# Kernel tuning notes

Measured on AMD Instinct MI355X. Metric: run time of the kernel, lower is better.

## Reference

```python
import jax, jax.numpy as jnp
import numpy as np

V, E = 1024, 2048
IN_DIM = OUT_DIM = 256
H = 4
D = OUT_DIM // H           # head_dim = 64
ENC = 8                    # causal_encoding_dim
HID = 32                   # causal_gate_hidden
LN_EPS = 1e-5


def setup_inputs() -> dict:
    key = jax.random.key(0)
    ks = jax.random.split(key, 12)
    s = 0.05
    return {
        "h": jax.random.normal(ks[0], (V, IN_DIM), jnp.float32),
        "causal_effects": jax.random.normal(ks[1], (V, V, 2), jnp.float32),
        "W": jax.random.normal(ks[2], (IN_DIM, OUT_DIM), jnp.float32) * s,
        "attn_w": jax.random.normal(ks[3], (2 * D + ENC,), jnp.float32) * s,
        "enc_w": jax.random.normal(ks[4], (2, ENC), jnp.float32) * s,
        "enc_b": jnp.zeros((ENC,), jnp.float32),
        "g1_w": jax.random.normal(ks[5], (2, HID), jnp.float32) * s,
        "g1_b": jnp.zeros((HID,), jnp.float32),
        "g2_w": jax.random.normal(ks[6], (HID, 1), jnp.float32) * s,
        "g2_b": jnp.zeros((1,), jnp.float32),
        "ln_g": jnp.ones((OUT_DIM,), jnp.float32),
        "ln_b": jnp.zeros((OUT_DIM,), jnp.float32),
        "incidence": jax.random.randint(ks[7], (V, E), 0, 2, dtype=jnp.int32),
    }


def _chan_forward(h, causal_effects, W, attn_w, enc_w, enc_b,
                  g1_w, g1_b, g2_w, g2_b, ln_g, ln_b, incidence):
    num_v, num_e = incidence.shape
    M = (incidence > 0).astype(h.dtype)                 # [V,E] binary membership
    mask = incidence > 0                                 # [V,E] bool

    Wh = h @ W                                           # [V,O]
    Whh = Wh.reshape(num_v, H, D)                        # [V,H,D]

    cnt_e = M.sum(axis=0)                                # [E] edge sizes
    deg_e = jnp.maximum(cnt_e, 1.0)
    h_bar = (M.T @ Wh) / deg_e[:, None]                  # [E,O] edge means
    hbh = h_bar.reshape(num_e, H, D)                     # [E,H,D]

    # number of "other" members for each (v,e): |e| - [v in e]
    n_ve = cnt_e[None, :] - M                            # [V,E]
    inv_n = jnp.where(n_ve > 0, 1.0 / jnp.maximum(n_ve, 1.0), 0.0)

    # per-(v,e) mean causal effect over other members of e
    diag_ce = jnp.diagonal(causal_effects, axis1=0, axis2=1).T   # [V,2]
    S = jnp.einsum('vuk,ue->vek', causal_effects, M)             # sum over members
    S = S - M[:, :, None] * diag_ce[:, None, :]                  # exclude u==v
    ce_mean = S * inv_n[:, :, None]                              # [V,E,2] (0 if no others)

    c = ce_mean @ enc_w + enc_b                                  # [V,E,ENC]

    a_v, a_e, a_c = attn_w[:D], attn_w[D:2 * D], attn_w[2 * D:]
    scores = (jnp.einsum('vhd,d->vh', Whh, a_v)[:, None, :]
              + jnp.einsum('ehd,d->eh', hbh, a_e)[None, :, :]
              + (c @ a_c)[:, :, None])                           # [V,E,H]
    scores = jax.nn.leaky_relu(scores, 0.2)
    neg = jnp.asarray(-1e9, scores.dtype)
    scores = jnp.where(mask[:, :, None], scores, neg)
    alpha = jax.nn.softmax(scores, axis=1) * mask[:, :, None].astype(scores.dtype)
    ap = alpha * inv_n[:, :, None]                               # alpha / n_others

    # causal gate psi(v,u) in [0,1], per vertex pair
    z = jax.nn.relu(causal_effects @ g1_w + g1_b)                # [V,V,HID]
    G = jax.nn.sigmoid((z @ g2_w)[..., 0] + g2_b[0])             # [V,V]

    # spread attention over edge members: A[v,u,h] = sum_e ap[v,e,h] * M[u,e]
    A = jnp.einsum('veh,ue->vuh', ap, M)                         # [V,V,H]
    out = jnp.einsum('vuh,vu,uhd->vhd', A, G, Whh)               # gated messages
    # remove self-contribution (u == v)
    s_v = ap.sum(axis=1)                                         # [V,H]
    Gvv = jnp.diagonal(G)                                        # [V]
    out = out - s_v[:, :, None] * Gvv[:, None, None] * Whh       # [V,H,D]

    out = out.reshape(num_v, -1) + Wh                            # residual (in==out dim)
    mu = out.mean(axis=-1, keepdims=True)
    var = out.var(axis=-1, keepdims=True)
    out = (out - mu) / jnp.sqrt(var + LN_EPS) * ln_g + ln_b
    return out                                                   # dropout = identity (eval)


def reference(h, causal_effects, W, attn_w, enc_w, enc_b,
              g1_w, g1_b, g2_w, g2_b, ln_g, ln_b, incidence):
    return _chan_forward(h, causal_effects, W, attn_w, enc_w, enc_b,
                         g1_w, g1_b, g2_w, g2_b, ln_g, ln_b, incidence)
```

## Files before the change

### kernel.cpp

```cpp
#include <hip/hip_runtime.h>
#include <hip/hip_bf16.h>

#define NV 1024
#define NE 2048

typedef unsigned short u16;
typedef unsigned char u8;
typedef unsigned long long u64;
typedef __attribute__((ext_vector_type(8))) short bf16x8;
typedef __attribute__((ext_vector_type(4))) float f32x4;
typedef __attribute__((ext_vector_type(16))) float f32x16;
typedef __attribute__((ext_vector_type(2))) long i64x2;

__device__ __forceinline__ float bf2f(u16 u) { return __uint_as_float(((unsigned)u) << 16); }
__device__ __forceinline__ u16 f2bf(float f) {
  unsigned x = __float_as_uint(f);
  return (u16)((x + 0x7fffu + ((x >> 16) & 1u)) >> 16);
}
__device__ __forceinline__ u8 f2fp8(float f) {
  unsigned x = __float_as_uint(f);
  unsigned sgn = (x >> 24) & 0x80;
  float af = __uint_as_float(x & 0x7fffffff);
  unsigned q;
  if (af >= 448.f) {
    q = 0x7e;
  } else if (af < 0.015625f) {
    q = (unsigned)rintf(af * 512.f);
  } else {
    unsigned xa = x & 0x7fffffff;
    xa += 0x7ffff + ((xa >> 20) & 1);
    q = (xa >> 20) - 960;
    if (q > 0x7e) q = 0x7e;
  }
  return (u8)(sgn | q);
}

#define GLL(src, dst)                                                        \
  __builtin_amdgcn_global_load_lds(                                          \
      (const __attribute__((address_space(1))) void*)(src),                  \
      (__attribute__((address_space(3))) void*)(dst), 16, 0, 0)

template <int N>
__device__ __forceinline__ void waitcnt_vm() {
  if constexpr (N == 0) asm volatile("s_waitcnt vmcnt(0)" ::: "memory");
  else if constexpr (N == 3) asm volatile("s_waitcnt vmcnt(3)" ::: "memory");
  else if constexpr (N == 8) asm volatile("s_waitcnt vmcnt(8)" ::: "memory");
}
__device__ __forceinline__ void waitcnt_lgkm0() {
  asm volatile("s_waitcnt lgkmcnt(0)" ::: "memory");
}
__device__ __forceinline__ void barrier_raw() { __builtin_amdgcn_s_barrier(); }

__device__ __forceinline__ void invswz(int g, int& row, int& kq) {
  int pb = g * 16;
  int lb = pb ^ ((((pb >> 8) & 1) << 6) | (((pb >> 7) & 1) << 5) |
                 ((((pb >> 6) ^ (pb >> 8)) & 1) << 4));
  row = lb >> 6;
  kq = lb & 63;
}
__device__ __forceinline__ int fwdswz(int la) { return la ^ (((la >> 6) & 7) << 4); }

template <int EPI>
__global__ __launch_bounds__(128) void mfma8_w2(
    const u8* __restrict__ A, int lda, long sA,
    const u8* __restrict__ BT, int ldb, long sBT,
    void* __restrict__ Cp, int ldc, long sC, int K, float unsc,
    const float* __restrict__ Gm) {
  __shared__ __align__(16) char L[32768];
  const int t = threadIdx.x;
  const int wave = t >> 6, lane = t & 63;
  const int l31 = lane & 31, lh = lane >> 5;
  const int m0 = blockIdx.x * 64, n0 = blockIdx.y * 64;
  const int zz = blockIdx.z;
  const u8* Ab = A + sA * zz;
  const u8* Bb = BT + sBT * zz;

  char* Lw = L + wave * 16384;
  char* A0 = Lw;
  char* B0 = Lw + 4096;
  char* A1 = Lw + 8192;
  char* B1 = Lw + 12288;

  int rL[4], qL[4];
#pragma unroll
  for (int j = 0; j < 4; j++) invswz(j * 64 + lane, rL[j], qL[j]);

  f32x16 acc[2][2] = {};

  auto stage = [&](char* Ad, char* Bd, int tile) {
    waitcnt_lgkm0();
    const long kb = (long)tile * 64;
#pragma unroll
    for (int j = 0; j < 4; j++)
      GLL(Ab + (long)(m0 + rL[j]) * lda + kb + qL[j], Ad + j * 1024);
#pragma unroll
    for (int j = 0; j < 4; j++)
      GLL(Bb + (long)(n0 + rL[j]) * ldb + kb + qL[j], Bd + j * 1024);
  };
  auto comp = [&](const char* A_, const char* B_) {
#pragma unroll
    for (int kss2 = 0; kss2 < 2; kss2++) {
      i64x2 av[2], bv[2];
#pragma unroll
      for (int mi = 0; mi < 2; mi++)
        av[mi] = *(const i64x2*)(A_ + fwdswz((mi * 32 + l31) * 64 + kss2 * 32 + lh * 16));
#pragma unroll
      for (int ni = 0; ni < 2; ni++)
        bv[ni] = *(const i64x2*)(B_ + fwdswz((ni * 32 + l31) * 64 + kss2 * 32 + lh * 16));
#pragma unroll
      for (int mi = 0; mi < 2; mi++)
#pragma unroll
        for (int ni = 0; ni < 2; ni++) {
          acc[mi][ni] = __builtin_amdgcn_mfma_f32_32x32x16_fp8_fp8(
              av[mi][0], bv[ni][0], acc[mi][ni], 0, 0, 0);
          acc[mi][ni] = __builtin_amdgcn_mfma_f32_32x32x16_fp8_fp8(
              av[mi][1], bv[ni][1], acc[mi][ni], 0, 0, 0);
        }
    }
  };

  const int nt2 = K / 128;
  const int tb = wave * nt2;
  stage(A0, B0, tb);
  for (int i = 0; i + 2 < nt2; i += 2) {
    stage(A1, B1, tb + i + 1);
    waitcnt_vm<8>();
    comp(A0, B0);
    stage(A0, B0, tb + i + 2);
    waitcnt_vm<8>();
    comp(A1, B1);
  }
  stage(A1, B1, tb + nt2 - 1);
  waitcnt_vm<8>();
  comp(A0, B0);
  waitcnt_vm<0>();
  comp(A1, B1);

  waitcnt_lgkm0();
  float4* myD = (float4*)Lw;
  const float* otD = (const float*)(L + (wave ^ 1) * 16384);
  if (wave == 0) {
#pragma unroll
    for (int ni = 0; ni < 2; ni++)
#pragma unroll
      for (int r4 = 0; r4 < 4; r4++)
        myD[r4 * 128 + ni * 64 + lane] =
            make_float4(acc[1][ni][r4 * 4 + 0], acc[1][ni][r4 * 4 + 1],
                        acc[1][ni][r4 * 4 + 2], acc[1][ni][r4 * 4 + 3]);
  } else {
#pragma unroll
    for (int ni = 0; ni < 2; ni++)
#pragma unroll
      for (int r4 = 0; r4 < 4; r4++)
        myD[r4 * 128 + ni * 64 + lane] =
            make_float4(acc[0][ni][r4 * 4 + 0], acc[0][ni][r4 * 4 + 1],
                        acc[0][ni][r4 * 4 + 2], acc[0][ni][r4 * 4 + 3]);
  }
  __syncthreads();

  auto store_one = [&](int m, int n, float vv) {
    if constexpr (EPI == 0) {
      ((float*)Cp)[sC * zz + (long)m * ldc + n] = vv * unsc;
    } else {
      ((u16*)Cp)[sC * zz + (long)m * ldc + n] = f2bf(vv * unsc * Gm[(long)m * NV + n]);
    }
  };
  if (wave == 0) {
#pragma unroll
    for (int ni = 0; ni < 2; ni++)
#pragma unroll
      for (int r = 0; r < 16; r++) {
        float vv = acc[0][ni][r] + otD[((r >> 2) * 128 + ni * 64 + lane) * 4 + (r & 3)];
        int m = m0 + (r & 3) + 8 * (r >> 2) + 4 * lh;
        store_one(m, n0 + ni * 32 + l31, vv);
      }
  } else {
#pragma unroll
    for (int ni = 0; ni < 2; ni++)
#pragma unroll
      for (int r = 0; r < 16; r++) {
        float vv = acc[1][ni][r] + otD[((r >> 2) * 128 + ni * 64 + lane) * 4 + (r & 3)];
        int m = m0 + 32 + (r & 3) + 8 * (r >> 2) + 4 * lh;
        store_one(m, n0 + ni * 32 + l31, vv);
      }
  }
}

__global__ __launch_bounds__(256) void mfma_bt8(
    const u16* __restrict__ A, const u16* __restrict__ BT,
    float* __restrict__ Cp) {
  constexpr int FM = 4, FN = 2;
  __shared__ __align__(16) char As0[8192];
  __shared__ __align__(16) char As1[8192];
  __shared__ __align__(16) char Bs0[4096];
  __shared__ __align__(16) char Bs1[4096];
  const int t = threadIdx.x;
  const int wave = t >> 6, lane = t & 63;
  const int lhi = lane >> 4, llo = lane & 15;
  const int wm = (wave >> 1) * 64, wn = (wave & 1) * 32;
  const int m0 = blockIdx.y * 128;
  const int zz = blockIdx.z >> 3, ks = blockIdx.z & 7;
  const char* Ab = (const char*)(A + (long)NV * NV * zz + ks * 128);
  const char* Bb = (const char*)(BT + (long)64 * NV * zz + ks * 128);
  const long lda2 = (long)NV * 2, ldb2 = (long)NV * 2;

  int rA0, qA0, rA1, qA1;
  invswz(t, rA0, qA0);
  invswz(t + 256, rA1, qA1);
  const int wofs = (t & 192) * 16;

  f32x4 acc[FM][FN] = {};

  auto stage = [&](char* Ad, char* Bd, int k0) {
    const long kb = (long)k0 * 2;
    GLL(Ab + (long)(m0 + rA0) * lda2 + kb + qA0, Ad + wofs);
    GLL(Ab + (long)(m0 + rA1) * lda2 + kb + qA1, Ad + 4096 + wofs);
    GLL(Bb + (long)rA0 * ldb2 + kb + qA0, Bd + wofs);
  };
  auto compute = [&](const char* A_, const char* B_) {
    bf16x8 af[FM], bfv[FN];
#pragma unroll
    for (int mi = 0; mi < FM; mi++)
      af[mi] = *(const bf16x8*)(A_ + fwdswz((wm + mi * 16 + llo) * 64 + lhi * 16));
#pragma unroll
    for (int ni = 0; ni < FN; ni++)
      bfv[ni] = *(const bf16x8*)(B_ + fwdswz((wn + ni * 16 + llo) * 64 + lhi * 16));
#pragma unroll
    for (int mi = 0; mi < FM; mi++)
#pragma unroll
      for (int ni = 0; ni < FN; ni++)
        acc[mi][ni] =
            __builtin_amdgcn_mfma_f32_16x16x32_bf16(af[mi], bfv[ni], acc[mi][ni], 0, 0, 0);
  };

  stage(As0, Bs0, 0);
  stage(As1, Bs1, 32);
  waitcnt_vm<3>();
  barrier_raw();
  compute(As0, Bs0);
  barrier_raw();
  stage(As0, Bs0, 64);
  waitcnt_vm<3>();
  barrier_raw();
  compute(As1, Bs1);
  barrier_raw();
  stage(As1, Bs1, 96);
  waitcnt_vm<3>();
  barrier_raw();
  compute(As0, Bs0);
  waitcnt_vm<0>();
  barrier_raw();
  compute(As1, Bs1);

#pragma unroll
  for (int mi = 0; mi < FM; mi++)
#pragma unroll
    for (int ni = 0; ni < FN; ni++)
#pragma unroll
      for (int r = 0; r < 4; r++) {
        int m = m0 + wm + mi * 16 + lhi * 4 + r;
        int n = wn + ni * 16 + llo;
        Cp[(long)ks * (NV * 256) + (long)m * 256 + zz * 64 + n] = acc[mi][ni][r];
      }
}

__global__ __launch_bounds__(256) void mm_f32(
    const float* __restrict__ Ap, const float* __restrict__ Bp,
    float* __restrict__ Cp) {
  __shared__ float As[16][68];
  __shared__ float Bs[16][68];
  const int t = threadIdx.x;
  const int tx = t & 15, ty = t >> 4;
  const int m0 = blockIdx.y * 64, n0 = blockIdx.x * 64;
  const int lr = t >> 2, lc4 = (t & 3) * 4;
  const int bk = t >> 4, bn = (t & 15) * 4;
  float acc[4][4] = {};
  for (int k0 = 0; k0 < 256; k0 += 16) {
    float4 a4 = *(const float4*)(Ap + (long)(m0 + lr) * 256 + k0 + lc4);
    As[lc4 + 0][lr] = a4.x;
    As[lc4 + 1][lr] = a4.y;
    As[lc4 + 2][lr] = a4.z;
    As[lc4 + 3][lr] = a4.w;
    float4 b4 = *(const float4*)(Bp + (long)(k0 + bk) * 256 + n0 + bn);
    Bs[bk][bn + 0] = b4.x;
    Bs[bk][bn + 1] = b4.y;
    Bs[bk][bn + 2] = b4.z;
    Bs[bk][bn + 3] = b4.w;
    __syncthreads();
#pragma unroll
    for (int kk = 0; kk < 16; kk++) {
      float a[4], b[4];
      *(float4*)a = *(const float4*)&As[kk][ty * 4];
      *(float4*)b = *(const float4*)&Bs[kk][tx * 4];
#pragma unroll
      for (int i = 0; i < 4; i++)
#pragma unroll
        for (int j = 0; j < 4; j++) acc[i][j] = fmaf(a[i], b[j], acc[i][j]);
    }
    __syncthreads();
  }
#pragma unroll
  for (int i = 0; i < 4; i++)
#pragma unroll
    for (int j = 0; j < 4; j++)
      Cp[(long)(m0 + ty * 4 + i) * 256 + n0 + tx * 4 + j] = acc[i][j];
}

__global__ __launch_bounds__(256) void k_conv(const int* __restrict__ inc,
                                              const float* __restrict__ qe,
                                              u8* __restrict__ Mbf,
                                              u8* __restrict__ Mtbf,
                                              float* __restrict__ part) {
  __shared__ u8 tile[64][68];
  const int e0 = blockIdx.x * 64, v0 = blockIdx.y * 64;
  const int t = threadIdx.x;
#pragma unroll
  for (int p = 0; p < 4; p++) {
    int r = p * 16 + (t >> 4);
    int c4 = (t & 15) * 4;
    int4 q = *(const int4*)(inc + (long)(v0 + r) * NE + e0 + c4);
    uchar4 w;
    w.x = q.x > 0 ? 0x38 : 0;
    w.y = q.y > 0 ? 0x38 : 0;
    w.z = q.z > 0 ? 0x38 : 0;
    w.w = q.w > 0 ? 0x38 : 0;
    *(uchar4*)&Mbf[(long)(v0 + r) * NE + e0 + c4] = w;
    tile[c4 + 0][r] = w.x;
    tile[c4 + 1][r] = w.y;
    tile[c4 + 2][r] = w.z;
    tile[c4 + 3][r] = w.w;
  }
  __syncthreads();
#pragma unroll
  for (int p = 0; p < 4; p++) {
    int er = p * 16 + (t >> 4);
    int vc4 = (t & 15) * 4;
    uchar4 w;
    w.x = tile[er][vc4 + 0];
    w.y = tile[er][vc4 + 1];
    w.z = tile[er][vc4 + 2];
    w.w = tile[er][vc4 + 3];
    *(uchar4*)&Mtbf[(long)(e0 + er) * NV + v0 + vc4] = w;
  }
  int er = t >> 2, q4 = t & 3;
  float c = 0, s0 = 0, s1 = 0, s2 = 0, s3 = 0;
  for (int vl = q4 * 16; vl < q4 * 16 + 16; vl++) {
    if (tile[er][vl]) {
      c += 1.f;
      const float* q4p = &qe[(long)(v0 + vl) * 4];
      s0 += q4p[0];
      s1 += q4p[1];
      s2 += q4p[2];
      s3 += q4p[3];
    }
  }
#pragma unroll
  for (int m = 1; m <= 2; m <<= 1) {
    c += __shfl_xor(c, m);
    s0 += __shfl_xor(s0, m);
    s1 += __shfl_xor(s1, m);
    s2 += __shfl_xor(s2, m);
    s3 += __shfl_xor(s3, m);
  }
  if (q4 == 0) {
    int b = blockIdx.y;
    int e = e0 + er;
    part[(0 * 16 + b) * NE + e] = c;
    part[(1 * 16 + b) * NE + e] = s0;
    part[(2 * 16 + b) * NE + e] = s1;
    part[(3 * 16 + b) * NE + e] = s2;
    part[(4 * 16 + b) * NE + e] = s3;
  }
}

__global__ __launch_bounds__(256) void k_trw(const float* __restrict__ Wh,
                                             u16* __restrict__ Whht) {
  __shared__ u16 tile[64][65];
  const int c0 = blockIdx.x * 64, v0 = blockIdx.y * 64;
  const int t = threadIdx.x;
#pragma unroll
  for (int p = 0; p < 4; p++) {
    int r = p * 16 + (t >> 4);
    int c4 = (t & 15) * 4;
    float4 q = *(const float4*)(Wh + (long)(v0 + r) * 256 + c0 + c4);
    tile[c4 + 0][r] = f2bf(q.x);
    tile[c4 + 1][r] = f2bf(q.y);
    tile[c4 + 2][r] = f2bf(q.z);
    tile[c4 + 3][r] = f2bf(q.w);
  }
  __syncthreads();
#pragma unroll
  for (int p = 0; p < 4; p++) {
    int cr = p * 16 + (t >> 4);
    int vc4 = (t & 15) * 4;
    ushort4 w;
    w.x = tile[cr][vc4 + 0];
    w.y = tile[cr][vc4 + 1];
    w.z = tile[cr][vc4 + 2];
    w.w = tile[cr][vc4 + 3];
    *(ushort4*)&Whht[(long)(c0 + cr) * NV + v0 + vc4] = w;
  }
}

__global__ __launch_bounds__(256) void k_qse1(const float* __restrict__ Wh,
                                              const float* __restrict__ attn_w,
                                              float* __restrict__ qv, float* __restrict__ qe) {
  int v = blockIdx.x, t = threadIdx.x;
  int d = t & 63, h = t >> 6;
  float x = Wh[(long)v * 256 + t];
  float pv = x * attn_w[d];
  float pe = x * attn_w[64 + d];
  for (int s = 32; s; s >>= 1) {
    pv += __shfl_down(pv, s);
    pe += __shfl_down(pe, s);
  }
  if (d == 0) {
    qv[v * 4 + h] = pv;
    qe[v * 4 + h] = pe;
  }
}

__global__ __launch_bounds__(256) void k_sered(const float* __restrict__ part,
                                               float* __restrict__ cnt, float* __restrict__ se) {
  int e = blockIdx.x * 256 + threadIdx.x;
  int j = blockIdx.y;
  float s = 0;
  for (int b = 0; b < 16; b++) s += part[(j * 16 + b) * NE + e];
  if (j == 0)
    cnt[e] = s;
  else
    se[e * 4 + (j - 1)] = s;
}

__global__ __launch_bounds__(256) void k_G(const float* __restrict__ ce,
                                           const float* __restrict__ enc_w,
                                           const float* __restrict__ attn_w,
                                           const float* __restrict__ g1w,
                                           const float* __restrict__ g1b,
                                           const float* __restrict__ g2w,
                                           const float* __restrict__ g2b,
                                           float* __restrict__ G, u8* __restrict__ wce) {
  long idx = (long)blockIdx.x * 256 + threadIdx.x;
  float2 c = *(const float2*)(ce + idx * 2);
  float ew0 = 0, ew1 = 0;
#pragma unroll
  for (int j = 0; j < 8; j++) {
    float ac = attn_w[128 + j];
    ew0 += enc_w[j] * ac;
    ew1 += enc_w[8 + j] * ac;
  }
  wce[idx] = f2fp8((c.x * ew0 + c.y * ew1) * 512.f);
  float s = g2b[0];
#pragma unroll
  for (int j = 0; j < 32; j++) {
    float zz = fmaxf(c.x * g1w[j] + c.y * g1w[32 + j] + g1b[j], 0.f);
    s = fmaf(zz, g2w[j], s);
  }
  G[idx] = 1.f / (1.f + expf(-s));
}

__global__ __launch_bounds__(256) void k_softmax(
    const float* __restrict__ P, const u8* __restrict__ Mbf, const float* __restrict__ cnt,
    const float* __restrict__ qv, const float* __restrict__ se, const float* __restrict__ ce,
    const float* __restrict__ enc_w, const float* __restrict__ attn_w,
    const float* __restrict__ enc_b, u8* __restrict__ ap, float* __restrict__ sv) {
  int v = blockIdx.x, t = threadIdx.x;
  float ew0 = 0, ew1 = 0, ebac = 0;
#pragma unroll
  for (int j = 0; j < 8; j++) {
    float ac = attn_w[128 + j];
    ew0 += enc_w[j] * ac;
    ew1 += enc_w[8 + j] * ac;
    ebac += enc_b[j] * ac;
  }
  float dce = ce[((long)v * NV + v) * 2] * ew0 + ce[((long)v * NV + v) * 2 + 1] * ew1;
  float svh[4];
#pragma unroll
  for (int hh = 0; hh < 4; hh++) svh[hh] = qv[v * 4 + hh];

  const int e0 = t * 8;
  u64 mb = *(const u64*)(Mbf + (long)v * NE + e0);
  float pv8[8], cn8[8];
  *(float4*)&pv8[0] = *(const float4*)(P + (long)v * NE + e0);
  *(float4*)&pv8[4] = *(const float4*)(P + (long)v * NE + e0 + 4);
  *(float4*)&cn8[0] = *(const float4*)(cnt + e0);
  *(float4*)&cn8[4] = *(const float4*)(cnt + e0 + 4);
  float se8[8][4];
#pragma unroll
  for (int i = 0; i < 8; i++) *(float4*)&se8[i][0] = *(const float4*)(se + (long)(e0 + i) * 4);

  float sc[8][4];
  float invn[8], msk[8];
  float mx[4] = {-3e38f, -3e38f, -3e38f, -3e38f};
#pragma unroll
  for (int i = 0; i < 8; i++) {
    float cnte = cn8[i];
    float mask = ((mb >> (8 * i)) & 0xff) ? 1.f : 0.f;
    float nve = cnte - mask;
    float inv = nve > 0.f ? 1.f / nve : 0.f;
    float rdg = 1.f / fmaxf(cnte, 1.f);
    invn[i] = inv;
    msk[i] = mask;
    float cc = inv * (pv8[i] - mask * dce) + ebac;
#pragma unroll
    for (int hh = 0; hh < 4; hh++) {
      float s = svh[hh] + se8[i][hh] * rdg + cc;
      s = s > 0.f ? s : 0.2f * s;
      s = mask > 0.f ? s : -1e9f;
      sc[i][hh] = s;
      mx[hh] = fmaxf(mx[hh], s);
    }
  }
  __shared__ float red[4][256];
#pragma unroll
  for (int hh = 0; hh < 4; hh++) red[hh][t] = mx[hh];
  __syncthreads();
  for (int s = 128; s; s >>= 1) {
    if (t < s)
#pragma unroll
      for (int hh = 0; hh < 4; hh++) red[hh][t] = fmaxf(red[hh][t], red[hh][t + s]);
    __syncthreads();
  }
  float gm[4];
#pragma unroll
  for (int hh = 0; hh < 4; hh++) gm[hh] = red[hh][0];
  __syncthreads();

  float lsum[4] = {0, 0, 0, 0};
#pragma unroll
  for (int i = 0; i < 8; i++)
#pragma unroll
    for (int hh = 0; hh < 4; hh++) {
      float p = expf(sc[i][hh] - gm[hh]);
      sc[i][hh] = p;
      lsum[hh] += p;
    }
#pragma unroll
  for (int hh = 0; hh < 4; hh++) red[hh][t] = lsum[hh];
  __syncthreads();
  for (int s = 128; s; s >>= 1) {
    if (t < s)
#pragma unroll
      for (int hh = 0; hh < 4; hh++) red[hh][t] += red[hh][t + s];
    __syncthreads();
  }
  float inv_s[4];
#pragma unroll
  for (int hh = 0; hh < 4; hh++) inv_s[hh] = 1.f / red[hh][0];
  __syncthreads();

  float lsv[4] = {0, 0, 0, 0};
#pragma unroll
  for (int hh = 0; hh < 4; hh++) {
    u64 packed = 0;
#pragma unroll
    for (int i = 0; i < 8; i++) {
      float a = sc[i][hh] * inv_s[hh] * msk[i] * invn[i];
      packed |= (u64)f2fp8(a * 131072.f) << (8 * i);
      lsv[hh] += a;
    }
    *(u64*)(ap + (long)hh * NV * NE + (long)v * NE + e0) = packed;
  }
#pragma unroll
  for (int hh = 0; hh < 4; hh++) red[hh][t] = lsv[hh];
  __syncthreads();
  for (int s = 128; s; s >>= 1) {
    if (t < s)
#pragma unroll
      for (int hh = 0; hh < 4; hh++) red[hh][t] += red[hh][t + s];
    __syncthreads();
  }
  if (t == 0)
#pragma unroll
    for (int hh = 0; hh < 4; hh++) sv[v * 4 + hh] = red[hh][0];
}

__global__ __launch_bounds__(256) void k_redln(
    const float* __restrict__ part, const float* __restrict__ Wh,
    const float* __restrict__ G, const float* __restrict__ sv,
    const float* __restrict__ lng, const float* __restrict__ lnb,
    float* __restrict__ out) {
  int v = blockIdx.x, t = threadIdx.x;
  float x = 0.f;
#pragma unroll
  for (int s = 0; s < 8; s++) x += part[(long)s * NV * 256 + (long)v * 256 + t];
  int z = t >> 6;
  float corr = 1.f - sv[v * 4 + z] * G[(long)v * NV + v];
  x += Wh[(long)v * 256 + t] * corr;
  __shared__ float red[256];
  red[t] = x;
  __syncthreads();
  for (int s = 128; s; s >>= 1) {
    if (t < s) red[t] += red[t + s];
    __syncthreads();
  }
  float mu = red[0] * (1.f / 256.f);
  __syncthreads();
  float d = x - mu;
  red[t] = d * d;
  __syncthreads();
  for (int s = 128; s; s >>= 1) {
    if (t < s) red[t] += red[t + s];
    __syncthreads();
  }
  float var = red[0] * (1.f / 256.f);
  out[(long)v * 256 + t] = d / sqrtf(var + 1e-5f) * lng[t] + lnb[t];
}

extern "C" void kernel_launch(void* const* d_in, const int* in_sizes, int n_in,
                              void* d_out, int out_size, void* d_ws, size_t ws_size,
                              hipStream_t stream) {
  const float* h = (const float*)d_in[0];
  const float* ce = (const float*)d_in[1];
  const float* W = (const float*)d_in[2];
  const float* attn_w = (const float*)d_in[3];
  const float* enc_w = (const float*)d_in[4];
  const float* enc_b = (const float*)d_in[5];
  const float* g1w = (const float*)d_in[6];
  const float* g1b = (const float*)d_in[7];
  const float* g2w = (const float*)d_in[8];
  const float* g2b = (const float*)d_in[9];
  const float* lng = (const float*)d_in[10];
  const float* lnb = (const float*)d_in[11];
  const int* inc = (const int*)d_in[12];
  float* out = (float*)d_out;

  size_t off = 0;
  char* base = (char*)d_ws;
  auto alloc = [&](size_t bytes) {
    void* p = base + off;
    off += (bytes + 255) & ~(size_t)255;
    return p;
  };
  float* Wh = (float*)alloc((size_t)NV * 256 * 4);
  float* cnt = (float*)alloc((size_t)NE * 4);
  float* qv = (float*)alloc((size_t)NV * 4 * 4);
  float* qe = (float*)alloc((size_t)NV * 4 * 4);
  float* se = (float*)alloc((size_t)NE * 4 * 4);
  float* sv = (float*)alloc((size_t)NV * 4 * 4);
  float* G = (float*)alloc((size_t)NV * NV * 4);
  u8* wce = (u8*)alloc((size_t)NV * NV);
  u8* Mbf = (u8*)alloc((size_t)NV * NE);
  u16* Whht = (u16*)alloc((size_t)256 * NV * 2);
  float* P = (float*)alloc((size_t)NV * NE * 4);
  u8* ap = (u8*)alloc((size_t)4 * NV * NE);
  u16* Bh = (u16*)alloc((size_t)4 * NV * NV * 2);
  float* part = P;
  u8* Mtbf = (u8*)Bh;
  float* part8 = P;
  (void)ws_size;
  (void)in_sizes;
  (void)n_in;
  (void)out_size;

  mm_f32<<<dim3(256 / 64, NV / 64), 256, 0, stream>>>(h, W, Wh);
  k_trw<<<dim3(256 / 64, NV / 64), 256, 0, stream>>>(Wh, Whht);
  k_qse1<<<NV, 256, 0, stream>>>(Wh, attn_w, qv, qe);
  k_conv<<<dim3(NE / 64, NV / 64), 256, 0, stream>>>(inc, qe, Mbf, Mtbf, part);
  k_sered<<<dim3(NE / 256, 5), 256, 0, stream>>>(part, cnt, se);
  k_G<<<(NV * NV) / 256, 256, 0, stream>>>(ce, enc_w, attn_w, g1w, g1b, g2w, g2b, G, wce);
  mfma8_w2<0><<<dim3(NV / 64, NE / 64, 1), 128, 0, stream>>>(
      wce, NV, 0, Mtbf, NV, 0, P, NE, 0, NV, 1.f / 512.f, nullptr);
  k_softmax<<<NV, 256, 0, stream>>>(P, Mbf, cnt, qv, se, ce, enc_w, attn_w, enc_b, ap, sv);
  mfma8_w2<1><<<dim3(NV / 64, NV / 64, 4), 128, 0, stream>>>(
      ap, NE, (long)NV * NE, Mbf, NE, 0, Bh, NV, (long)NV * NV, NE, 1.f / 131072.f, G);
  mfma_bt8<<<dim3(1, NV / 128, 32), 256, 0, stream>>>(Bh, Whht, part8);
  k_redln<<<NV, 256, 0, stream>>>(part8, Wh, G, sv, lng, lnb, out);
}
```

Baseline: 100.8 us.

## Fuse Wh transpose into matmul, store P as bf16, use wave-shuffle softmax reductions

Folds the bf16 transpose of Wh into the epilogue of the fp32 matmul, which removes one kernel launch and a re-read of Wh. The fp8 GEMM's EPI==0 epilogue now writes P as bf16 instead of fp32, halving that intermediate's traffic, and the softmax kernel reads it as bf16. The softmax block reductions switch from shared-memory tree loops with many barriers to wave shuffles plus a small cross-wave combine, and expf becomes __expf. The price is lower precision in P and in the exponentials.

```diff
diff --git a/kernel.cpp b/kernel.cpp
--- a/kernel.cpp
+++ b/kernel.cpp
@@ -160,7 +160,7 @@
 
   auto store_one = [&](int m, int n, float vv) {
     if constexpr (EPI == 0) {
-      ((float*)Cp)[sC * zz + (long)m * ldc + n] = vv * unsc;
+      ((u16*)Cp)[sC * zz + (long)m * ldc + n] = f2bf(vv * unsc);
     } else {
       ((u16*)Cp)[sC * zz + (long)m * ldc + n] = f2bf(vv * unsc * Gm[(long)m * NV + n]);
     }
@@ -266,9 +266,10 @@
 
 __global__ __launch_bounds__(256) void mm_f32(
     const float* __restrict__ Ap, const float* __restrict__ Bp,
-    float* __restrict__ Cp) {
+    float* __restrict__ Cp, u16* __restrict__ Whht) {
   __shared__ float As[16][68];
   __shared__ float Bs[16][68];
+  __shared__ u16 ttile[64][68];
   const int t = threadIdx.x;
   const int tx = t & 15, ty = t >> 4;
   const int m0 = blockIdx.y * 64, n0 = blockIdx.x * 64;
@@ -302,8 +303,17 @@
 #pragma unroll
   for (int i = 0; i < 4; i++)
 #pragma unroll
-    for (int j = 0; j < 4; j++)
+    for (int j = 0; j < 4; j++) {
       Cp[(long)(m0 + ty * 4 + i) * 256 + n0 + tx * 4 + j] = acc[i][j];
+      ttile[tx * 4 + j][ty * 4 + i] = f2bf(acc[i][j]);
+    }
+  __syncthreads();
+  const int cr = t >> 2, vc = (t & 3) * 16;
+#pragma unroll
+  for (int q = 0; q < 4; q++) {
+    ushort4 w = *(const ushort4*)&ttile[cr][vc + q * 4];
+    *(ushort4*)&Whht[(long)(n0 + cr) * NV + m0 + vc + q * 4] = w;
+  }
 }
 
 __global__ __launch_bounds__(256) void k_conv(const int* __restrict__ inc,
@@ -373,35 +383,6 @@
   }
 }
 
-__global__ __launch_bounds__(256) void k_trw(const float* __restrict__ Wh,
-                                             u16* __restrict__ Whht) {
-  __shared__ u16 tile[64][65];
-  const int c0 = blockIdx.x * 64, v0 = blockIdx.y * 64;
-  const int t = threadIdx.x;
-#pragma unroll
-  for (int p = 0; p < 4; p++) {
-    int r = p * 16 + (t >> 4);
-    int c4 = (t & 15) * 4;
-    float4 q = *(const float4*)(Wh + (long)(v0 + r) * 256 + c0 + c4);
-    tile[c4 + 0][r] = f2bf(q.x);
-    tile[c4 + 1][r] = f2bf(q.y);
-    tile[c4 + 2][r] = f2bf(q.z);
-    tile[c4 + 3][r] = f2bf(q.w);
-  }
-  __syncthreads();
-#pragma unroll
-  for (int p = 0; p < 4; p++) {
-    int cr = p * 16 + (t >> 4);
-    int vc4 = (t & 15) * 4;
-    ushort4 w;
-    w.x = tile[cr][vc4 + 0];
-    w.y = tile[cr][vc4 + 1];
-    w.z = tile[cr][vc4 + 2];
-    w.w = tile[cr][vc4 + 3];
-    *(ushort4*)&Whht[(long)(c0 + cr) * NV + v0 + vc4] = w;
-  }
-}
-
 __global__ __launch_bounds__(256) void k_qse1(const float* __restrict__ Wh,
                                               const float* __restrict__ attn_w,
                                               float* __restrict__ qv, float* __restrict__ qe) {
@@ -456,15 +437,16 @@
     float zz = fmaxf(c.x * g1w[j] + c.y * g1w[32 + j] + g1b[j], 0.f);
     s = fmaf(zz, g2w[j], s);
   }
-  G[idx] = 1.f / (1.f + expf(-s));
+  G[idx] = 1.f / (1.f + __expf(-s));
 }
 
 __global__ __launch_bounds__(256) void k_softmax(
-    const float* __restrict__ P, const u8* __restrict__ Mbf, const float* __restrict__ cnt,
+    const u16* __restrict__ P, const u8* __restrict__ Mbf, const float* __restrict__ cnt,
     const float* __restrict__ qv, const float* __restrict__ se, const float* __restrict__ ce,
     const float* __restrict__ enc_w, const float* __restrict__ attn_w,
     const float* __restrict__ enc_b, u8* __restrict__ ap, float* __restrict__ sv) {
   int v = blockIdx.x, t = threadIdx.x;
+  const int wave = t >> 6, lane = t & 63;
   float ew0 = 0, ew1 = 0, ebac = 0;
 #pragma unroll
   for (int j = 0; j < 8; j++) {
@@ -480,9 +462,11 @@
 
   const int e0 = t * 8;
   u64 mb = *(const u64*)(Mbf + (long)v * NE + e0);
+  ushort4 pb0 = *(const ushort4*)(P + (long)v * NE + e0);
+  ushort4 pb1 = *(const ushort4*)(P + (long)v * NE + e0 + 4);
   float pv8[8], cn8[8];
-  *(float4*)&pv8[0] = *(const float4*)(P + (long)v * NE + e0);
-  *(float4*)&pv8[4] = *(const float4*)(P + (long)v * NE + e0 + 4);
+  pv8[0] = bf2f(pb0.x); pv8[1] = bf2f(pb0.y); pv8[2] = bf2f(pb0.z); pv8[3] = bf2f(pb0.w);
+  pv8[4] = bf2f(pb1.x); pv8[5] = bf2f(pb1.y); pv8[6] = bf2f(pb1.z); pv8[7] = bf2f(pb1.w);
   *(float4*)&cn8[0] = *(const float4*)(cnt + e0);
   *(float4*)&cn8[4] = *(const float4*)(cnt + e0 + 4);
   float se8[8][4];
@@ -511,43 +495,41 @@
       mx[hh] = fmaxf(mx[hh], s);
     }
   }
-  __shared__ float red[4][256];
-#pragma unroll
-  for (int hh = 0; hh < 4; hh++) red[hh][t] = mx[hh];
-  __syncthreads();
-  for (int s = 128; s; s >>= 1) {
-    if (t < s)
-#pragma unroll
-      for (int hh = 0; hh < 4; hh++) red[hh][t] = fmaxf(red[hh][t], red[hh][t + s]);
-    __syncthreads();
-  }
+  __shared__ float redM[4][4], redS[4][4], redV[4][4];
+#pragma unroll
+  for (int hh = 0; hh < 4; hh++) {
+    float x = mx[hh];
+#pragma unroll
+    for (int m = 1; m <= 32; m <<= 1) x = fmaxf(x, __shfl_xor(x, m));
+    if (lane == 0) redM[hh][wave] = x;
+  }
+  __syncthreads();
   float gm[4];
 #pragma unroll
-  for (int hh = 0; hh < 4; hh++) gm[hh] = red[hh][0];
-  __syncthreads();
+  for (int hh = 0; hh < 4; hh++)
+    gm[hh] = fmaxf(fmaxf(redM[hh][0], redM[hh][1]), fmaxf(redM[hh][2], redM[hh][3]));
 
   float lsum[4] = {0, 0, 0, 0};
 #pragma unroll
   for (int i = 0; i < 8; i++)
 #pragma unroll
     for (int hh = 0; hh < 4; hh++) {
-      float p = expf(sc[i][hh] - gm[hh]);
+      float p = __expf(sc[i][hh] - gm[hh]);
       sc[i][hh] = p;
       lsum[hh] += p;
     }
 #pragma unroll
-  for (int hh = 0; hh < 4; hh++) red[hh][t] = lsum[hh];
-  __syncthreads();
-  for (int s = 128; s; s >>= 1) {
-    if (t < s)
-#pragma unroll
-      for (int hh = 0; hh < 4; hh++) red[hh][t] += red[hh][t + s];
-    __syncthreads();
-  }
+  for (int hh = 0; hh < 4; hh++) {
+    float x = lsum[hh];
+#pragma unroll
+    for (int m = 1; m <= 32; m <<= 1) x += __shfl_xor(x, m);
+    if (lane == 0) redS[hh][wave] = x;
+  }
+  __syncthreads();
   float inv_s[4];
 #pragma unroll
-  for (int hh = 0; hh < 4; hh++) inv_s[hh] = 1.f / red[hh][0];
-  __syncthreads();
+  for (int hh = 0; hh < 4; hh++)
+    inv_s[hh] = 1.f / (redS[hh][0] + redS[hh][1] + redS[hh][2] + redS[hh][3]);
 
   float lsv[4] = {0, 0, 0, 0};
 #pragma unroll
@@ -562,17 +544,17 @@
     *(u64*)(ap + (long)hh * NV * NE + (long)v * NE + e0) = packed;
   }
 #pragma unroll
-  for (int hh = 0; hh < 4; hh++) red[hh][t] = lsv[hh];
-  __syncthreads();
-  for (int s = 128; s; s >>= 1) {
-    if (t < s)
-#pragma unroll
-      for (int hh = 0; hh < 4; hh++) red[hh][t] += red[hh][t + s];
-    __syncthreads();
-  }
+  for (int hh = 0; hh < 4; hh++) {
+    float x = lsv[hh];
+#pragma unroll
+    for (int m = 1; m <= 32; m <<= 1) x += __shfl_xor(x, m);
+    if (lane == 0) redV[hh][wave] = x;
+  }
+  __syncthreads();
   if (t == 0)
 #pragma unroll
-    for (int hh = 0; hh < 4; hh++) sv[v * 4 + hh] = red[hh][0];
+    for (int hh = 0; hh < 4; hh++)
+      sv[v * 4 + hh] = redV[hh][0] + redV[hh][1] + redV[hh][2] + redV[hh][3];
 }
 
 __global__ __launch_bounds__(256) void k_redln(
@@ -642,19 +624,19 @@
   u8* wce = (u8*)alloc((size_t)NV * NV);
   u8* Mbf = (u8*)alloc((size_t)NV * NE);
   u16* Whht = (u16*)alloc((size_t)256 * NV * 2);
-  float* P = (float*)alloc((size_t)NV * NE * 4);
+  float* Pr = (float*)alloc((size_t)NV * NE * 4);
   u8* ap = (u8*)alloc((size_t)4 * NV * NE);
   u16* Bh = (u16*)alloc((size_t)4 * NV * NV * 2);
-  float* part = P;
+  u16* P = (u16*)Pr;
+  float* part = Pr;
   u8* Mtbf = (u8*)Bh;
-  float* part8 = P;
+  float* part8 = Pr;
   (void)ws_size;
   (void)in_sizes;
   (void)n_in;
   (void)out_size;
 
-  mm_f32<<<dim3(256 / 64, NV / 64), 256, 0, stream>>>(h, W, Wh);
-  k_trw<<<dim3(256 / 64, NV / 64), 256, 0, stream>>>(Wh, Whht);
+  mm_f32<<<dim3(256 / 64, NV / 64), 256, 0, stream>>>(h, W, Wh, Whht);
   k_qse1<<<NV, 256, 0, stream>>>(Wh, attn_w, qv, qe);
   k_conv<<<dim3(NE / 64, NV / 64), 256, 0, stream>>>(inc, qe, Mbf, Mtbf, part);
   k_sered<<<dim3(NE / 256, 5), 256, 0, stream>>>(part, cnt, se);
```

New measurement: 93.77 us. 1.07x faster.
